# Kernel tuning notes

Hardware: AMD Instinct MI355X
Metric: run time of the kernel (lower is better)

Reference implementation:

```python
import jax, jax.numpy as jnp
import numpy as np

NUM_HEADS = 8
NUM_GROUPS = 32
EPS = 1e-5


def setup_inputs() -> dict:
    key = jax.random.key(0)
    ks = jax.random.split(key, 7)
    B, C, H, W = 16, 512, 32, 32
    x = jax.random.normal(ks[0], (B, C, H, W), dtype=jnp.float32)
    gn_gamma = jnp.ones((C,), dtype=jnp.float32)
    gn_beta = jnp.zeros((C,), dtype=jnp.float32)
    # Conv1d with kernel_size=1 is a per-position matmul: weight [out, in]
    qkv_w = jax.random.normal(ks[1], (3 * C, C), dtype=jnp.float32) / np.sqrt(C)
    qkv_b = jax.random.normal(ks[2], (3 * C,), dtype=jnp.float32) * 0.01
    proj_w = jax.random.normal(ks[3], (C, C), dtype=jnp.float32) / np.sqrt(C)
    proj_b = jax.random.normal(ks[4], (C,), dtype=jnp.float32) * 0.01
    return {"x": x, "gn_gamma": gn_gamma, "gn_beta": gn_beta,
            "qkv_w": qkv_w, "qkv_b": qkv_b, "proj_w": proj_w, "proj_b": proj_b}


def group_norm(x, gamma, beta):
    # x: [B, C, H, W]
    B, C, H, W = x.shape
    xg = x.reshape(B, NUM_GROUPS, C // NUM_GROUPS, H, W)
    mean = xg.mean(axis=(2, 3, 4), keepdims=True)
    var = xg.var(axis=(2, 3, 4), keepdims=True)
    xg = (xg - mean) * jax.lax.rsqrt(var + EPS)
    x = xg.reshape(B, C, H, W)
    return x * gamma[None, :, None, None] + beta[None, :, None, None]


def reference(x, gn_gamma, gn_beta, qkv_w, qkv_b, proj_w, proj_b):
    B, C, H, W = x.shape
    N = H * W
    hd = C // NUM_HEADS  # head dim
    h = group_norm(x, gn_gamma, gn_beta).reshape(B, C, N)
    # 1x1 Conv1d == matmul over channel dim
    qkv = jnp.einsum('oc,bcn->bon', qkv_w, h) + qkv_b[None, :, None]
    qkv = qkv.reshape(B, 3, NUM_HEADS, hd, N)
    q, k, v = qkv[:, 0], qkv[:, 1], qkv[:, 2]  # each [B, h, d, N]
    scale = hd ** (-0.5)
    attn = jnp.einsum('bhdn,bhdm->bhnm', q, k) * scale  # [B, h, N, N]
    attn = jax.nn.softmax(attn, axis=-1)
    out = jnp.einsum('bhnm,bhdm->bhdn', attn, v).reshape(B, C, N)
    out = jnp.einsum('oc,bcn->bon', proj_w, out) + proj_b[None, :, None]
    return x + out.reshape(B, C, H, W)
```

## Files before the change

kernel.cpp:

```cpp
#include <hip/hip_runtime.h>

typedef unsigned short u16;
typedef unsigned int u32;
typedef __bf16 bf16x8 __attribute__((ext_vector_type(8)));
typedef float f32x4 __attribute__((ext_vector_type(4)));
typedef float f32x16 __attribute__((ext_vector_type(16)));

#define B_ 16
#define C_ 512
#define N_ 1024
#define NB_ 16384
#define K_ 512
#define M3_ 1536
#define SCALE_Q 0.18033688011112042f

__device__ __forceinline__ u16 f2bf(float f) {
  u32 u = __float_as_uint(f);
  u32 r = (u + 0x7FFFu + ((u >> 16) & 1u)) >> 16;
  return (u16)r;
}

__device__ __forceinline__ void gl_lds16(const void* g, void* l) {
  __builtin_amdgcn_global_load_lds(
      (const __attribute__((address_space(1))) u32*)(uintptr_t)g,
      (__attribute__((address_space(3))) u32*)(u32)(uintptr_t)l, 16, 0, 0);
}

__device__ __forceinline__ u32 cvtpk(float lo, float hi) {
  u32 r;
  asm("v_cvt_pk_bf16_f32 %0, %1, %2" : "=v"(r) : "v"(lo), "v"(hi));
  return r;
}

__device__ __forceinline__ float exp2a(float x) {
  float r;
  asm("v_exp_f32 %0, %1" : "=v"(r) : "v"(x));
  return r;
}

__device__ __forceinline__ void plswap2(u32& a, u32& b) {
#if __has_builtin(__builtin_amdgcn_permlane32_swap)
  auto r = __builtin_amdgcn_permlane32_swap((int)a, (int)b, false, false);
  a = (u32)r[0];
  b = (u32)r[1];
#else
  asm("v_permlane32_swap_b32 %0, %1" : "+v"(a), "+v"(b));
#endif
}

__device__ __forceinline__ float xhalf_sum(float x) {
  u32 a = __float_as_uint(x), b = a;
  plswap2(a, b);
  return __uint_as_float(a) + __uint_as_float(b);
}

__global__ __launch_bounds__(256) void cast_bf16_kernel(const float* __restrict__ src,
                                                        u16* __restrict__ dst, int n) {
  int i = blockIdx.x * 256 + threadIdx.x;
  if (i < n) dst[i] = f2bf(src[i]);
}

__global__ __launch_bounds__(256) void gnorm_kernel(const float* __restrict__ x,
                                                    const float* __restrict__ gamma,
                                                    const float* __restrict__ beta,
                                                    u16* __restrict__ ht) {
  int blk = blockIdx.x;
  int b = blk >> 5, g = blk & 31;
  int t = threadIdx.x;
  const float* xb = x + ((size_t)(b * C_ + g * 16) << 10);
  float v[16][4];
  float s = 0.f, sq = 0.f;
#pragma unroll
  for (int cc = 0; cc < 16; ++cc) {
#pragma unroll
    for (int r = 0; r < 4; ++r) {
      float f = xb[cc * 1024 + r * 256 + t];
      v[cc][r] = f; s += f; sq += f * f;
    }
  }
#pragma unroll
  for (int m = 32; m >= 1; m >>= 1) { s += __shfl_xor(s, m, 64); sq += __shfl_xor(sq, m, 64); }
  __shared__ float red[8];
  int w = t >> 6;
  if ((t & 63) == 0) { red[w * 2] = s; red[w * 2 + 1] = sq; }
  __syncthreads();
  s = red[0] + red[2] + red[4] + red[6];
  sq = red[1] + red[3] + red[5] + red[7];
  float mean = s * (1.f / 16384.f);
  float var = sq * (1.f / 16384.f) - mean * mean;
  float rstd = rsqrtf(var + 1e-5f);
  float gm[16], bt[16];
#pragma unroll
  for (int cc = 0; cc < 16; ++cc) {
    gm[cc] = gamma[g * 16 + cc] * rstd;
    bt[cc] = beta[g * 16 + cc];
  }
  u16* hb = ht + ((size_t)(b << 10)) * C_ + g * 16;
#pragma unroll
  for (int r = 0; r < 4; ++r) {
    u32 pk[8];
#pragma unroll
    for (int q = 0; q < 8; ++q) {
      float f0 = (v[2 * q][r] - mean) * gm[2 * q] + bt[2 * q];
      float f1 = (v[2 * q + 1][r] - mean) * gm[2 * q + 1] + bt[2 * q + 1];
      pk[q] = (u32)f2bf(f0) | ((u32)f2bf(f1) << 16);
    }
    u16* dp = hb + (size_t)(r * 256 + t) * C_;
    uint4 a = {pk[0], pk[1], pk[2], pk[3]};
    uint4 b4 = {pk[4], pk[5], pk[6], pk[7]};
    *(uint4*)dp = a;
    *(uint4*)(dp + 8) = b4;
  }
}

template <int EPI>
__global__ __launch_bounds__(256) void gemm_kernel(const u16* __restrict__ A,
                                                   const u16* __restrict__ BT,
                                                   const float* __restrict__ bias,
                                                   u16* __restrict__ Co,
                                                   u16* __restrict__ qTo,
                                                   u16* __restrict__ kTo,
                                                   const float* __restrict__ xres,
                                                   float* __restrict__ Fo) {
  __shared__ u16 ldsA[128 * 64];
  __shared__ u16 ldsB[128 * 64];
  int t = threadIdx.x;
  int l = t & 63, w = t >> 6;
  int wr = w >> 1, wc = w & 1;
  int ro0 = blockIdx.y * 128, co0 = blockIdx.x * 128;
  f32x4 acc[4][4];
#pragma unroll
  for (int m = 0; m < 4; ++m)
#pragma unroll
    for (int n = 0; n < 4; ++n) acc[m][n] = {0.f, 0.f, 0.f, 0.f};
  int srow = t >> 3, sg = t & 7;
  for (int kt = 0; kt < 8; ++kt) {
    int k0 = kt * 64;
#pragma unroll
    for (int i = 0; i < 4; ++i) {
      int row = i * 32 + srow;
      int gl = sg ^ (row & 7);
      gl_lds16(A + (size_t)(ro0 + row) * K_ + k0 + gl * 8, ldsA + (i * 32 + w * 8) * 64);
      gl_lds16(BT + (size_t)(co0 + row) * K_ + k0 + gl * 8, ldsB + (i * 32 + w * 8) * 64);
    }
    __syncthreads();
#pragma unroll
    for (int ks = 0; ks < 2; ++ks) {
      bf16x8 af[4], bfr[4];
#pragma unroll
      for (int m = 0; m < 4; ++m) {
        int row = wr * 64 + m * 16 + (l & 15);
        int ph = (ks * 4 + (l >> 4)) ^ (row & 7);
        af[m] = *(const bf16x8*)&ldsA[row * 64 + ph * 8];
      }
#pragma unroll
      for (int n = 0; n < 4; ++n) {
        int row = wc * 64 + n * 16 + (l & 15);
        int ph = (ks * 4 + (l >> 4)) ^ (row & 7);
        bfr[n] = *(const bf16x8*)&ldsB[row * 64 + ph * 8];
      }
#pragma unroll
      for (int m = 0; m < 4; ++m)
#pragma unroll
        for (int n = 0; n < 4; ++n)
          acc[m][n] = __builtin_amdgcn_mfma_f32_16x16x32_bf16(af[m], bfr[n], acc[m][n], 0, 0, 0);
    }
    __syncthreads();
  }
  if (EPI == 0 && ro0 < 1024) {
    int sel = ro0 >> 9;
    u16* dstb = sel ? kTo : qTo;
    float scl = sel ? 1.f : SCALE_Q;
#pragma unroll
    for (int m = 0; m < 4; ++m) {
      int row0 = ro0 + wr * 64 + m * 16 + (l >> 4) * 4;
      int o = row0 & 511;
      int h = o >> 6, d0 = o & 63;
      float bv0 = bias[row0], bv1 = bias[row0 + 1];
      float bv2 = bias[row0 + 2], bv3 = bias[row0 + 3];
#pragma unroll
      for (int n = 0; n < 4; ++n) {
        int col = co0 + wc * 64 + n * 16 + (l & 15);
        int bb = col >> 10, nn = col & 1023;
        float v0 = (acc[m][n][0] + bv0) * scl;
        float v1 = (acc[m][n][1] + bv1) * scl;
        float v2 = (acc[m][n][2] + bv2) * scl;
        float v3 = (acc[m][n][3] + bv3) * scl;
        uint2 ov = {cvtpk(v0, v1), cvtpk(v2, v3)};
        *(uint2*)(dstb + ((size_t)((bb * 8 + h) << 10) + nn) * 64 + d0) = ov;
      }
    }
  } else {
#pragma unroll
    for (int m = 0; m < 4; ++m) {
#pragma unroll
      for (int j = 0; j < 4; ++j) {
        int row = ro0 + wr * 64 + m * 16 + (l >> 4) * 4 + j;
        float bv = bias[row];
#pragma unroll
        for (int n = 0; n < 4; ++n) {
          int col = co0 + wc * 64 + n * 16 + (l & 15);
          float val = acc[m][n][j] + bv;
          if (EPI == 0) {
            Co[(size_t)row * NB_ + col] = f2bf(val);
          } else {
            int bb = col >> 10, nn = col & 1023;
            size_t oi = (((size_t)(bb * C_ + row)) << 10) + nn;
            Fo[oi] = xres[oi] + val;
          }
        }
      }
    }
  }
}

__global__ __launch_bounds__(256) void attn_kernel(const u16* __restrict__ qT,
                                                   const u16* __restrict__ kT,
                                                   const u16* __restrict__ qkv,
                                                   u16* __restrict__ aoT) {
  __shared__ u16 KV[2][4096];
  int bid = blockIdx.x;
  int wid = (bid & 7) * 128 + (bid >> 3);
  int qt2 = wid & 7, h = (wid >> 3) & 7, b = wid >> 6;
  int bh = b * 8 + h;
  int t = threadIdx.x, l = t & 63, w = t >> 6;
  int lq = l & 31, hi = l >> 5;
  int q0 = qt2 * 128 + w * 32;

  const u16* qbase = qT + ((size_t)(bh << 10) + q0 + lq) * 64 + hi * 8;
  bf16x8 qf[4];
#pragma unroll
  for (int kc = 0; kc < 4; ++kc) qf[kc] = *(const bf16x8*)(qbase + kc * 16);

  f32x16 accO[2];
#pragma unroll
  for (int dt = 0; dt < 2; ++dt)
#pragma unroll
    for (int r = 0; r < 16; ++r) accO[dt][r] = 0.f;
  float lsum = 0.f;

  const u16 *src0, *src1;
  u32 ldso0, ldso1;
  int adv;
  if (w < 2) {
    int i0 = 2 * w, i1 = 2 * w + 1;
    src0 = kT + ((size_t)(bh << 10) + i0 * 8 + (l >> 3)) * 64 + (((l & 7) ^ ((l >> 3) & 7)) * 8);
    src1 = kT + ((size_t)(bh << 10) + i1 * 8 + (l >> 3)) * 64 + (((l & 7) ^ ((l >> 3) & 7)) * 8);
    ldso0 = i0 * 512; ldso1 = i1 * 512;
    adv = 2048;
  } else {
    int j0 = 2 * (w - 2), j1 = 2 * (w - 2) + 1;
    src0 = qkv + (size_t)(2 * C_ + h * 64 + j0 * 16 + (l >> 2)) * NB_ + (b << 10) +
           (((l & 3) ^ ((l >> 3) & 3)) * 8);
    src1 = qkv + (size_t)(2 * C_ + h * 64 + j1 * 16 + (l >> 2)) * NB_ + (b << 10) +
           (((l & 3) ^ ((l >> 3) & 3)) * 8);
    ldso0 = 2048 + j0 * 512; ldso1 = 2048 + j1 * 512;
    adv = 32;
  }

  const u16* kfp[4];
#pragma unroll
  for (int kc = 0; kc < 4; ++kc)
    kfp[kc] = &KV[0][0] + lq * 64 + (((2 * kc + hi) ^ (lq & 7)) * 8);
  const u16* vfp[4];
#pragma unroll
  for (int dt = 0; dt < 2; ++dt)
#pragma unroll
    for (int kcc = 0; kcc < 2; ++kcc)
      vfp[dt * 2 + kcc] = &KV[0][0] + 2048 + (dt * 32 + lq) * 32 +
                          (((kcc * 2 + hi) ^ ((lq >> 1) & 3)) * 8);

  auto stage = [&](int buf) {
    gl_lds16(src0, &KV[buf][0] + ldso0);
    gl_lds16(src1, &KV[buf][0] + ldso1);
    src0 += adv;
    src1 += adv;
  };

  auto step = [&](int buf, bool dostage) {
    asm volatile("s_waitcnt vmcnt(0)" ::: "memory");
    __builtin_amdgcn_sched_barrier(0);
    __builtin_amdgcn_s_barrier();
    __builtin_amdgcn_sched_barrier(0);
    if (dostage) stage(buf ^ 1);
    bf16x8 kf[4];
#pragma unroll
    for (int kc = 0; kc < 4; ++kc) kf[kc] = *(const bf16x8*)(kfp[kc] + buf * 4096);
    f32x16 sc;
#pragma unroll
    for (int r = 0; r < 16; ++r) sc[r] = 0.f;
    __builtin_amdgcn_s_setprio(1);
#pragma unroll
    for (int kc = 0; kc < 4; ++kc)
      sc = __builtin_amdgcn_mfma_f32_32x32x16_bf16(kf[kc], qf[kc], sc, 0, 0, 0);
    __builtin_amdgcn_s_setprio(0);
    bf16x8 vf[4];
#pragma unroll
    for (int j = 0; j < 4; ++j) vf[j] = *(const bf16x8*)(vfp[j] + buf * 4096);
    float p0 = 0.f, p1 = 0.f, p2 = 0.f, p3 = 0.f;
#pragma unroll
    for (int r = 0; r < 4; ++r) {
      float e0 = exp2a(sc[4 * r + 0]);
      float e1 = exp2a(sc[4 * r + 1]);
      float e2 = exp2a(sc[4 * r + 2]);
      float e3 = exp2a(sc[4 * r + 3]);
      sc[4 * r + 0] = e0; sc[4 * r + 1] = e1;
      sc[4 * r + 2] = e2; sc[4 * r + 3] = e3;
      p0 += e0; p1 += e1; p2 += e2; p3 += e3;
    }
    lsum += (p0 + p1) + (p2 + p3);
    u32 pk[8];
#pragma unroll
    for (int p = 0; p < 8; ++p) pk[p] = cvtpk(sc[2 * p], sc[2 * p + 1]);
    u32 pfu[2][4];
#pragma unroll
    for (int cc = 0; cc < 2; ++cc) {
      u32 w0 = pk[cc * 4 + 0], w2 = pk[cc * 4 + 2];
      u32 w1 = pk[cc * 4 + 1], w3 = pk[cc * 4 + 3];
      plswap2(w0, w2);
      plswap2(w1, w3);
      pfu[cc][0] = w0; pfu[cc][1] = w1; pfu[cc][2] = w2; pfu[cc][3] = w3;
    }
    __builtin_amdgcn_s_setprio(1);
#pragma unroll
    for (int kcc = 0; kcc < 2; ++kcc)
#pragma unroll
      for (int dt = 0; dt < 2; ++dt) {
        union { u32 u[4]; bf16x8 v; } pf;
        pf.u[0] = pfu[kcc][0]; pf.u[1] = pfu[kcc][1];
        pf.u[2] = pfu[kcc][2]; pf.u[3] = pfu[kcc][3];
        accO[dt] = __builtin_amdgcn_mfma_f32_32x32x16_bf16(vf[dt * 2 + kcc], pf.v, accO[dt], 0, 0, 0);
      }
    __builtin_amdgcn_s_setprio(0);
  };

  stage(0);
#pragma unroll 1
  for (int s = 0; s < 15; ++s) {
    step(0, true);
    step(1, true);
  }
  step(0, true);
  step(1, false);

  float inv = 1.0f / xhalf_sum(lsum);
  u16* ob = aoT + ((size_t)((b << 10) + q0 + lq)) * C_ + h * 64;
#pragma unroll
  for (int dt = 0; dt < 2; ++dt)
#pragma unroll
    for (int rg = 0; rg < 4; ++rg) {
      int d0 = dt * 32 + rg * 8 + hi * 4;
      u32 w0 = cvtpk(accO[dt][rg * 4 + 0] * inv, accO[dt][rg * 4 + 1] * inv);
      u32 w1 = cvtpk(accO[dt][rg * 4 + 2] * inv, accO[dt][rg * 4 + 3] * inv);
      uint2 o = {w0, w1};
      *(uint2*)(ob + d0) = o;
    }
}

extern "C" void kernel_launch(void* const* d_in, const int* in_sizes, int n_in,
                              void* d_out, int out_size, void* d_ws, size_t ws_size,
                              hipStream_t stream) {
  const float* x = (const float*)d_in[0];
  const float* gamma = (const float*)d_in[1];
  const float* beta = (const float*)d_in[2];
  const float* qkv_w = (const float*)d_in[3];
  const float* qkv_b = (const float*)d_in[4];
  const float* proj_w = (const float*)d_in[5];
  const float* proj_b = (const float*)d_in[6];
  float* out = (float*)d_out;
  char* ws = (char*)d_ws;
  u16* wq = (u16*)(ws);
  u16* wp = (u16*)(ws + 1572864);
  u16* ht = (u16*)(ws + 2097152);
  u16* qkvo = (u16*)(ws + 18874368);
  u16* qT = (u16*)(ws + 69206016);
  u16* kT = (u16*)(ws + 85983232);
  u16* aoT = ht;

  cast_bf16_kernel<<<3072, 256, 0, stream>>>(qkv_w, wq, M3_ * K_);
  cast_bf16_kernel<<<1024, 256, 0, stream>>>(proj_w, wp, C_ * K_);
  gnorm_kernel<<<512, 256, 0, stream>>>(x, gamma, beta, ht);
  gemm_kernel<0><<<dim3(128, 12), 256, 0, stream>>>(wq, ht, qkv_b, qkvo, qT, kT, nullptr, nullptr);
  attn_kernel<<<1024, 256, 0, stream>>>(qT, kT, qkvo, aoT);
  gemm_kernel<1><<<dim3(128, 4), 256, 0, stream>>>(wp, aoT, proj_b, nullptr, nullptr, nullptr, x, out);
}
```

Baseline: 131.3 us.

## Triple-buffer GEMM LDS staging with async global-to-LDS prefetch pipeline

Replaces the single-buffered 64-wide K loop in the GEMM kernel with a three-stage ring of 32-wide K tiles. Loads for tile kt+2 are issued before computing tile kt, with explicit vmcnt waits and one barrier per iteration instead of two. The LDS swizzle is reworked for the 32-element row layout. LDS use rises from 32KB to 48KB per block, which may reduce occupancy, and the hand-written waitcnt sequencing is fragile.

```diff
diff --git a/kernel.cpp b/kernel.cpp
--- a/kernel.cpp
+++ b/kernel.cpp
@@ -122,8 +122,7 @@
                                                    u16* __restrict__ kTo,
                                                    const float* __restrict__ xres,
                                                    float* __restrict__ Fo) {
-  __shared__ u16 ldsA[128 * 64];
-  __shared__ u16 ldsB[128 * 64];
+  __shared__ __attribute__((aligned(16))) u16 lds[3][2][4096];
   int t = threadIdx.x;
   int l = t & 63, w = t >> 6;
   int wr = w >> 1, wc = w & 1;
@@ -133,40 +132,66 @@
   for (int m = 0; m < 4; ++m)
 #pragma unroll
     for (int n = 0; n < 4; ++n) acc[m][n] = {0.f, 0.f, 0.f, 0.f};
-  int srow = t >> 3, sg = t & 7;
-  for (int kt = 0; kt < 8; ++kt) {
-    int k0 = kt * 64;
-#pragma unroll
-    for (int i = 0; i < 4; ++i) {
-      int row = i * 32 + srow;
-      int gl = sg ^ (row & 7);
-      gl_lds16(A + (size_t)(ro0 + row) * K_ + k0 + gl * 8, ldsA + (i * 32 + w * 8) * 64);
-      gl_lds16(BT + (size_t)(co0 + row) * K_ + k0 + gl * 8, ldsB + (i * 32 + w * 8) * 64);
-    }
-    __syncthreads();
-#pragma unroll
-    for (int ks = 0; ks < 2; ++ks) {
-      bf16x8 af[4], bfr[4];
-#pragma unroll
-      for (int m = 0; m < 4; ++m) {
-        int row = wr * 64 + m * 16 + (l & 15);
-        int ph = (ks * 4 + (l >> 4)) ^ (row & 7);
-        af[m] = *(const bf16x8*)&ldsA[row * 64 + ph * 8];
-      }
-#pragma unroll
-      for (int n = 0; n < 4; ++n) {
-        int row = wc * 64 + n * 16 + (l & 15);
-        int ph = (ks * 4 + (l >> 4)) ^ (row & 7);
-        bfr[n] = *(const bf16x8*)&ldsB[row * 64 + ph * 8];
-      }
-#pragma unroll
-      for (int m = 0; m < 4; ++m)
-#pragma unroll
-        for (int n = 0; n < 4; ++n)
-          acc[m][n] = __builtin_amdgcn_mfma_f32_16x16x32_bf16(af[m], bfr[n], acc[m][n], 0, 0, 0);
-    }
-    __syncthreads();
-  }
+
+  int srow = w * 16 + (l >> 2);
+  int gsrc = (l ^ (l >> 2) ^ (l >> 4)) & 3;
+  const u16* srcA = A + (size_t)(ro0 + srow) * K_ + gsrc * 8;
+  const u16* srcB = BT + (size_t)(co0 + srow) * K_ + gsrc * 8;
+  u32 dsto = w * 512;
+
+  auto stage = [&](u16* bufA, u16* bufB, int kt) {
+    int k0 = kt * 32;
+    gl_lds16(srcA + k0, bufA + dsto);
+    gl_lds16(srcA + (size_t)64 * K_ + k0, bufA + dsto + 2048);
+    gl_lds16(srcB + k0, bufB + dsto);
+    gl_lds16(srcB + (size_t)64 * K_ + k0, bufB + dsto + 2048);
+  };
+
+  int slot = ((l >> 4) ^ (l & 3) ^ ((l >> 2) & 3)) & 3;
+  int aro = (wr * 64 + (l & 15)) * 32 + slot * 8;
+  int bro = (wc * 64 + (l & 15)) * 32 + slot * 8;
+
+  auto compute = [&](const u16* bufA, const u16* bufB) {
+    bf16x8 af[4], bfr[4];
+#pragma unroll
+    for (int m = 0; m < 4; ++m) af[m] = *(const bf16x8*)(bufA + aro + m * 512);
+#pragma unroll
+    for (int n = 0; n < 4; ++n) bfr[n] = *(const bf16x8*)(bufB + bro + n * 512);
+#pragma unroll
+    for (int m = 0; m < 4; ++m)
+#pragma unroll
+      for (int n = 0; n < 4; ++n)
+        acc[m][n] = __builtin_amdgcn_mfma_f32_16x16x32_bf16(af[m], bfr[n], acc[m][n], 0, 0, 0);
+  };
+
+  u16 *A0 = &lds[0][0][0], *B0 = &lds[0][1][0];
+  u16 *A1 = &lds[1][0][0], *B1 = &lds[1][1][0];
+  u16 *A2 = &lds[2][0][0], *B2 = &lds[2][1][0];
+  stage(A0, B0, 0);
+  stage(A1, B1, 1);
+#pragma unroll 1
+  for (int kt = 0; kt < 14; ++kt) {
+    asm volatile("s_waitcnt vmcnt(4)" ::: "memory");
+    __builtin_amdgcn_sched_barrier(0);
+    __builtin_amdgcn_s_barrier();
+    __builtin_amdgcn_sched_barrier(0);
+    stage(A2, B2, kt + 2);
+    compute(A0, B0);
+    u16* tp;
+    tp = A0; A0 = A1; A1 = A2; A2 = tp;
+    tp = B0; B0 = B1; B1 = B2; B2 = tp;
+  }
+  asm volatile("s_waitcnt vmcnt(4)" ::: "memory");
+  __builtin_amdgcn_sched_barrier(0);
+  __builtin_amdgcn_s_barrier();
+  __builtin_amdgcn_sched_barrier(0);
+  compute(A0, B0);
+  asm volatile("s_waitcnt vmcnt(0)" ::: "memory");
+  __builtin_amdgcn_sched_barrier(0);
+  __builtin_amdgcn_s_barrier();
+  __builtin_amdgcn_sched_barrier(0);
+  compute(A1, B1);
+
   if (EPI == 0 && ro0 < 1024) {
     int sel = ro0 >> 9;
     u16* dstb = sel ? kTo : qTo;
```

Measured after the change: 133.0 us. No clear change (+1.3%).

## Load K/V tiles directly from global into registers instead of LDS staging

Applied to the files above, without the earlier changes.

Removes the shared-memory double buffer and block barriers in the attention kernel. Each wave now loads its K and V MFMA fragments straight from global memory into registers, double-buffered across iterations. This removes the barrier synchronisation and LDS reads, but makes each of the four waves fetch the same K/V data independently, and the V loads become strided across rows.

```diff
diff --git a/kernel.cpp b/kernel.cpp
--- a/kernel.cpp
+++ b/kernel.cpp
@@ -218,7 +218,6 @@
                                                    const u16* __restrict__ kT,
                                                    const u16* __restrict__ qkv,
                                                    u16* __restrict__ aoT) {
-  __shared__ u16 KV[2][4096];
   int bid = blockIdx.x;
   int wid = (bid & 7) * 128 + (bid >> 3);
   int qt2 = wid & 7, h = (wid >> 3) & 7, b = wid >> 6;
@@ -239,53 +238,24 @@
     for (int r = 0; r < 16; ++r) accO[dt][r] = 0.f;
   float lsum = 0.f;
 
-  const u16 *src0, *src1;
-  u32 ldso0, ldso1;
-  int adv;
-  if (w < 2) {
-    int i0 = 2 * w, i1 = 2 * w + 1;
-    src0 = kT + ((size_t)(bh << 10) + i0 * 8 + (l >> 3)) * 64 + (((l & 7) ^ ((l >> 3) & 7)) * 8);
-    src1 = kT + ((size_t)(bh << 10) + i1 * 8 + (l >> 3)) * 64 + (((l & 7) ^ ((l >> 3) & 7)) * 8);
-    ldso0 = i0 * 512; ldso1 = i1 * 512;
-    adv = 2048;
-  } else {
-    int j0 = 2 * (w - 2), j1 = 2 * (w - 2) + 1;
-    src0 = qkv + (size_t)(2 * C_ + h * 64 + j0 * 16 + (l >> 2)) * NB_ + (b << 10) +
-           (((l & 3) ^ ((l >> 3) & 3)) * 8);
-    src1 = qkv + (size_t)(2 * C_ + h * 64 + j1 * 16 + (l >> 2)) * NB_ + (b << 10) +
-           (((l & 3) ^ ((l >> 3) & 3)) * 8);
-    ldso0 = 2048 + j0 * 512; ldso1 = 2048 + j1 * 512;
-    adv = 32;
-  }
-
-  const u16* kfp[4];
-#pragma unroll
-  for (int kc = 0; kc < 4; ++kc)
-    kfp[kc] = &KV[0][0] + lq * 64 + (((2 * kc + hi) ^ (lq & 7)) * 8);
-  const u16* vfp[4];
-#pragma unroll
-  for (int dt = 0; dt < 2; ++dt)
-#pragma unroll
-    for (int kcc = 0; kcc < 2; ++kcc)
-      vfp[dt * 2 + kcc] = &KV[0][0] + 2048 + (dt * 32 + lq) * 32 +
-                          (((kcc * 2 + hi) ^ ((lq >> 1) & 3)) * 8);
-
-  auto stage = [&](int buf) {
-    gl_lds16(src0, &KV[buf][0] + ldso0);
-    gl_lds16(src1, &KV[buf][0] + ldso1);
-    src0 += adv;
-    src1 += adv;
+  const u16* kfb = kT + ((size_t)(bh << 10) + lq) * 64 + hi * 8;
+  const u16* vfb = qkv + (size_t)(2 * C_ + h * 64 + lq) * NB_ + (b << 10) + hi * 8;
+
+  auto loadK = [&](bf16x8* dst, int mt) {
+    const u16* p = kfb + (size_t)(mt * 32) * 64;
+#pragma unroll
+    for (int kc = 0; kc < 4; ++kc) dst[kc] = *(const bf16x8*)(p + kc * 16);
   };
-
-  auto step = [&](int buf, bool dostage) {
-    asm volatile("s_waitcnt vmcnt(0)" ::: "memory");
-    __builtin_amdgcn_sched_barrier(0);
-    __builtin_amdgcn_s_barrier();
-    __builtin_amdgcn_sched_barrier(0);
-    if (dostage) stage(buf ^ 1);
-    bf16x8 kf[4];
-#pragma unroll
-    for (int kc = 0; kc < 4; ++kc) kf[kc] = *(const bf16x8*)(kfp[kc] + buf * 4096);
+  auto loadV = [&](bf16x8* dst, int mt) {
+    const u16* p = vfb + mt * 32;
+#pragma unroll
+    for (int dt = 0; dt < 2; ++dt)
+#pragma unroll
+      for (int kcc = 0; kcc < 2; ++kcc)
+        dst[dt * 2 + kcc] = *(const bf16x8*)(p + (size_t)(dt * 32) * NB_ + kcc * 16);
+  };
+
+  auto step = [&](const bf16x8* kf, const bf16x8* vf) {
     f32x16 sc;
 #pragma unroll
     for (int r = 0; r < 16; ++r) sc[r] = 0.f;
@@ -294,9 +264,6 @@
     for (int kc = 0; kc < 4; ++kc)
       sc = __builtin_amdgcn_mfma_f32_32x32x16_bf16(kf[kc], qf[kc], sc, 0, 0, 0);
     __builtin_amdgcn_s_setprio(0);
-    bf16x8 vf[4];
-#pragma unroll
-    for (int j = 0; j < 4; ++j) vf[j] = *(const bf16x8*)(vfp[j] + buf * 4096);
     float p0 = 0.f, p1 = 0.f, p2 = 0.f, p3 = 0.f;
 #pragma unroll
     for (int r = 0; r < 4; ++r) {
@@ -334,14 +301,18 @@
     __builtin_amdgcn_s_setprio(0);
   };
 
-  stage(0);
+  bf16x8 ka[4], va[4], kb[4], vb[4];
+  loadK(ka, 0); loadV(va, 0);
+  loadK(kb, 1); loadV(vb, 1);
 #pragma unroll 1
   for (int s = 0; s < 15; ++s) {
-    step(0, true);
-    step(1, true);
-  }
-  step(0, true);
-  step(1, false);
+    step(ka, va);
+    loadK(ka, 2 * s + 2); loadV(va, 2 * s + 2);
+    step(kb, vb);
+    loadK(kb, 2 * s + 3); loadV(vb, 2 * s + 3);
+  }
+  step(ka, va);
+  step(kb, vb);
 
   float inv = 1.0f / xhalf_sum(lsum);
   u16* ob = aoT + ((size_t)((b << 10) + q0 + lq)) * C_ + h * 64;
```

After: 201.8 us. 53.6% more time.

## Double attention KV tile to 64 keys, remap GEMM blocks per XCD, merge cast launches

Applied to the files above, without the earlier changes.

The attention kernel now stages 64 keys per step instead of 32, with a larger double-buffered LDS tile and two score MFMA chains per step. This halves the number of barrier and wait cycles and gives more independent MFMA work between them. The GEMM block index is remapped so that blocks on the same XCD share column tiles, aiming for better L2 reuse. The two weight-cast launches are merged into one kernel. The cost is doubled LDS use and more registers in the attention kernel, which could reduce occupancy.

```diff
diff --git a/kernel.cpp b/kernel.cpp
--- a/kernel.cpp
+++ b/kernel.cpp
@@ -54,10 +54,18 @@
   return __uint_as_float(a) + __uint_as_float(b);
 }
 
-__global__ __launch_bounds__(256) void cast_bf16_kernel(const float* __restrict__ src,
-                                                        u16* __restrict__ dst, int n) {
+__global__ __launch_bounds__(256) void cast2_kernel(const float* __restrict__ a,
+                                                    const float* __restrict__ b,
+                                                    u16* __restrict__ da,
+                                                    u16* __restrict__ db,
+                                                    int na, int nb) {
   int i = blockIdx.x * 256 + threadIdx.x;
-  if (i < n) dst[i] = f2bf(src[i]);
+  if (i < na) {
+    da[i] = f2bf(a[i]);
+  } else {
+    int j = i - na;
+    if (j < nb) db[j] = f2bf(b[j]);
+  }
 }
 
 __global__ __launch_bounds__(256) void gnorm_kernel(const float* __restrict__ x,
@@ -127,7 +135,11 @@
   int t = threadIdx.x;
   int l = t & 63, w = t >> 6;
   int wr = w >> 1, wc = w & 1;
-  int ro0 = blockIdx.y * 128, co0 = blockIdx.x * 128;
+  int lid = blockIdx.y * 128 + blockIdx.x;
+  int xcd = lid & 7, j2 = lid >> 3;
+  int bx = xcd * 16 + (j2 & 15);
+  int by = j2 >> 4;
+  int ro0 = by * 128, co0 = bx * 128;
   f32x4 acc[4][4];
 #pragma unroll
   for (int m = 0; m < 4; ++m)
@@ -218,7 +230,7 @@
                                                    const u16* __restrict__ kT,
                                                    const u16* __restrict__ qkv,
                                                    u16* __restrict__ aoT) {
-  __shared__ u16 KV[2][4096];
+  __shared__ u16 KV[2][8192];
   int bid = blockIdx.x;
   int wid = (bid & 7) * 128 + (bid >> 3);
   int qt2 = wid & 7, h = (wid >> 3) & 7, b = wid >> 6;
@@ -239,42 +251,41 @@
     for (int r = 0; r < 16; ++r) accO[dt][r] = 0.f;
   float lsum = 0.f;
 
-  const u16 *src0, *src1;
-  u32 ldso0, ldso1;
+  const u16* src;
+  u32 ldso;
+  size_t gstep;
   int adv;
   if (w < 2) {
-    int i0 = 2 * w, i1 = 2 * w + 1;
-    src0 = kT + ((size_t)(bh << 10) + i0 * 8 + (l >> 3)) * 64 + (((l & 7) ^ ((l >> 3) & 7)) * 8);
-    src1 = kT + ((size_t)(bh << 10) + i1 * 8 + (l >> 3)) * 64 + (((l & 7) ^ ((l >> 3) & 7)) * 8);
-    ldso0 = i0 * 512; ldso1 = i1 * 512;
-    adv = 2048;
+    src = kT + ((size_t)(bh << 10) + 32 * w + (l >> 3)) * 64 + (((l & 7) ^ ((l >> 3) & 7)) * 8);
+    ldso = 2048u * w;
+    gstep = 512;
+    adv = 4096;
   } else {
-    int j0 = 2 * (w - 2), j1 = 2 * (w - 2) + 1;
-    src0 = qkv + (size_t)(2 * C_ + h * 64 + j0 * 16 + (l >> 2)) * NB_ + (b << 10) +
-           (((l & 3) ^ ((l >> 3) & 3)) * 8);
-    src1 = qkv + (size_t)(2 * C_ + h * 64 + j1 * 16 + (l >> 2)) * NB_ + (b << 10) +
-           (((l & 3) ^ ((l >> 3) & 3)) * 8);
-    ldso0 = 2048 + j0 * 512; ldso1 = 2048 + j1 * 512;
-    adv = 32;
-  }
-
-  const u16* kfp[4];
-#pragma unroll
-  for (int kc = 0; kc < 4; ++kc)
-    kfp[kc] = &KV[0][0] + lq * 64 + (((2 * kc + hi) ^ (lq & 7)) * 8);
-  const u16* vfp[4];
+    src = qkv + (size_t)(2 * C_ + h * 64 + 32 * (w - 2) + (l >> 3)) * NB_ + (b << 10) +
+          (((l & 7) ^ ((l >> 3) & 7)) * 8);
+    ldso = 4096 + 2048u * (w - 2);
+    gstep = (size_t)8 * NB_;
+    adv = 64;
+  }
+
+  const u16* kfp[8];
+#pragma unroll
+  for (int c = 0; c < 2; ++c)
+#pragma unroll
+    for (int kc = 0; kc < 4; ++kc)
+      kfp[c * 4 + kc] = &KV[0][0] + (c * 32 + lq) * 64 + (((2 * kc + hi) ^ (lq & 7)) * 8);
+  const u16* vfp[8];
 #pragma unroll
   for (int dt = 0; dt < 2; ++dt)
 #pragma unroll
-    for (int kcc = 0; kcc < 2; ++kcc)
-      vfp[dt * 2 + kcc] = &KV[0][0] + 2048 + (dt * 32 + lq) * 32 +
-                          (((kcc * 2 + hi) ^ ((lq >> 1) & 3)) * 8);
+    for (int kcc = 0; kcc < 4; ++kcc)
+      vfp[dt * 4 + kcc] = &KV[0][0] + 4096 + (dt * 32 + lq) * 64 +
+                          (((2 * kcc + hi) ^ (lq & 7)) * 8);
 
   auto stage = [&](int buf) {
-    gl_lds16(src0, &KV[buf][0] + ldso0);
-    gl_lds16(src1, &KV[buf][0] + ldso1);
-    src0 += adv;
-    src1 += adv;
+#pragma unroll
+    for (int i = 0; i < 4; ++i) gl_lds16(src + i * gstep, &KV[buf][0] + ldso + i * 512);
+    src += adv;
   };
 
   auto step = [&](int buf, bool dostage) {
@@ -283,60 +294,79 @@
     __builtin_amdgcn_s_barrier();
     __builtin_amdgcn_sched_barrier(0);
     if (dostage) stage(buf ^ 1);
-    bf16x8 kf[4];
-#pragma unroll
-    for (int kc = 0; kc < 4; ++kc) kf[kc] = *(const bf16x8*)(kfp[kc] + buf * 4096);
-    f32x16 sc;
-#pragma unroll
-    for (int r = 0; r < 16; ++r) sc[r] = 0.f;
+    bf16x8 kf0[4], kf1[4];
+#pragma unroll
+    for (int kc = 0; kc < 4; ++kc) {
+      kf0[kc] = *(const bf16x8*)(kfp[kc] + buf * 8192);
+      kf1[kc] = *(const bf16x8*)(kfp[4 + kc] + buf * 8192);
+    }
+    f32x16 sc0, sc1;
+#pragma unroll
+    for (int r = 0; r < 16; ++r) { sc0[r] = 0.f; sc1[r] = 0.f; }
     __builtin_amdgcn_s_setprio(1);
 #pragma unroll
-    for (int kc = 0; kc < 4; ++kc)
-      sc = __builtin_amdgcn_mfma_f32_32x32x16_bf16(kf[kc], qf[kc], sc, 0, 0, 0);
+    for (int kc = 0; kc < 4; ++kc) {
+      sc0 = __builtin_amdgcn_mfma_f32_32x32x16_bf16(kf0[kc], qf[kc], sc0, 0, 0, 0);
+      sc1 = __builtin_amdgcn_mfma_f32_32x32x16_bf16(kf1[kc], qf[kc], sc1, 0, 0, 0);
+    }
     __builtin_amdgcn_s_setprio(0);
-    bf16x8 vf[4];
-#pragma unroll
-    for (int j = 0; j < 4; ++j) vf[j] = *(const bf16x8*)(vfp[j] + buf * 4096);
+    bf16x8 vf[8];
+#pragma unroll
+    for (int i = 0; i < 8; ++i) vf[i] = *(const bf16x8*)(vfp[i] + buf * 8192);
     float p0 = 0.f, p1 = 0.f, p2 = 0.f, p3 = 0.f;
 #pragma unroll
     for (int r = 0; r < 4; ++r) {
-      float e0 = exp2a(sc[4 * r + 0]);
-      float e1 = exp2a(sc[4 * r + 1]);
-      float e2 = exp2a(sc[4 * r + 2]);
-      float e3 = exp2a(sc[4 * r + 3]);
-      sc[4 * r + 0] = e0; sc[4 * r + 1] = e1;
-      sc[4 * r + 2] = e2; sc[4 * r + 3] = e3;
+      float e0 = exp2a(sc0[4 * r + 0]);
+      float e1 = exp2a(sc0[4 * r + 1]);
+      float e2 = exp2a(sc0[4 * r + 2]);
+      float e3 = exp2a(sc0[4 * r + 3]);
+      sc0[4 * r + 0] = e0; sc0[4 * r + 1] = e1;
+      sc0[4 * r + 2] = e2; sc0[4 * r + 3] = e3;
       p0 += e0; p1 += e1; p2 += e2; p3 += e3;
     }
+#pragma unroll
+    for (int r = 0; r < 4; ++r) {
+      float e0 = exp2a(sc1[4 * r + 0]);
+      float e1 = exp2a(sc1[4 * r + 1]);
+      float e2 = exp2a(sc1[4 * r + 2]);
+      float e3 = exp2a(sc1[4 * r + 3]);
+      sc1[4 * r + 0] = e0; sc1[4 * r + 1] = e1;
+      sc1[4 * r + 2] = e2; sc1[4 * r + 3] = e3;
+      p0 += e0; p1 += e1; p2 += e2; p3 += e3;
+    }
     lsum += (p0 + p1) + (p2 + p3);
-    u32 pk[8];
-#pragma unroll
-    for (int p = 0; p < 8; ++p) pk[p] = cvtpk(sc[2 * p], sc[2 * p + 1]);
-    u32 pfu[2][4];
-#pragma unroll
-    for (int cc = 0; cc < 2; ++cc) {
-      u32 w0 = pk[cc * 4 + 0], w2 = pk[cc * 4 + 2];
-      u32 w1 = pk[cc * 4 + 1], w3 = pk[cc * 4 + 3];
-      plswap2(w0, w2);
-      plswap2(w1, w3);
-      pfu[cc][0] = w0; pfu[cc][1] = w1; pfu[cc][2] = w2; pfu[cc][3] = w3;
-    }
-    __builtin_amdgcn_s_setprio(1);
-#pragma unroll
-    for (int kcc = 0; kcc < 2; ++kcc)
-#pragma unroll
-      for (int dt = 0; dt < 2; ++dt) {
+#pragma unroll
+    for (int c = 0; c < 2; ++c) {
+      const f32x16& scc = c ? sc1 : sc0;
+      u32 pk[8];
+#pragma unroll
+      for (int p = 0; p < 8; ++p) pk[p] = cvtpk(scc[2 * p], scc[2 * p + 1]);
+      u32 pfu[2][4];
+#pragma unroll
+      for (int cc = 0; cc < 2; ++cc) {
+        u32 w0 = pk[cc * 4 + 0], w2 = pk[cc * 4 + 2];
+        u32 w1 = pk[cc * 4 + 1], w3 = pk[cc * 4 + 3];
+        plswap2(w0, w2);
+        plswap2(w1, w3);
+        pfu[cc][0] = w0; pfu[cc][1] = w1; pfu[cc][2] = w2; pfu[cc][3] = w3;
+      }
+      __builtin_amdgcn_s_setprio(1);
+#pragma unroll
+      for (int cc = 0; cc < 2; ++cc) {
+        int kcc = c * 2 + cc;
         union { u32 u[4]; bf16x8 v; } pf;
-        pf.u[0] = pfu[kcc][0]; pf.u[1] = pfu[kcc][1];
-        pf.u[2] = pfu[kcc][2]; pf.u[3] = pfu[kcc][3];
-        accO[dt] = __builtin_amdgcn_mfma_f32_32x32x16_bf16(vf[dt * 2 + kcc], pf.v, accO[dt], 0, 0, 0);
-      }
-    __builtin_amdgcn_s_setprio(0);
+        pf.u[0] = pfu[cc][0]; pf.u[1] = pfu[cc][1];
+        pf.u[2] = pfu[cc][2]; pf.u[3] = pfu[cc][3];
+        accO[0] = __builtin_amdgcn_mfma_f32_32x32x16_bf16(vf[kcc], pf.v, accO[0], 0, 0, 0);
+        accO[1] = __builtin_amdgcn_mfma_f32_32x32x16_bf16(vf[4 + kcc], pf.v, accO[1], 0, 0, 0);
+      }
+      __builtin_amdgcn_s_setprio(0);
+    }
   };
 
   stage(0);
 #pragma unroll 1
-  for (int s = 0; s < 15; ++s) {
+  for (int s = 0; s < 7; ++s) {
     step(0, true);
     step(1, true);
   }
@@ -377,8 +407,7 @@
   u16* kT = (u16*)(ws + 85983232);
   u16* aoT = ht;
 
-  cast_bf16_kernel<<<3072, 256, 0, stream>>>(qkv_w, wq, M3_ * K_);
-  cast_bf16_kernel<<<1024, 256, 0, stream>>>(proj_w, wp, C_ * K_);
+  cast2_kernel<<<4096, 256, 0, stream>>>(qkv_w, proj_w, wq, wp, M3_ * K_, C_ * K_);
   gnorm_kernel<<<512, 256, 0, stream>>>(x, gamma, beta, ht);
   gemm_kernel<0><<<dim3(128, 12), 256, 0, stream>>>(wq, ht, qkv_b, qkvo, qT, kT, nullptr, nullptr);
   attn_kernel<<<1024, 256, 0, stream>>>(qT, kT, qkvo, aoT);
```

Result: no change. 130.4 us (-0.7%).
